# Kernel optimization log

Measured on AMD Instinct MI355X. Metric: run time of the kernel, lower is better.

Reference implementation:

```python
import jax, jax.numpy as jnp
import numpy as np
import math

B, N, DIM, H, D = 2, 2048, 1024, 16, 64
EXPECTED_K = 1.0
LAYERSCALE_INIT = 0.001
EPS = 1e-6  # flax LayerNorm default


def layer_norm(x, scale, bias):
    mu = jnp.mean(x, axis=-1, keepdims=True)
    var = jnp.mean((x - mu) ** 2, axis=-1, keepdims=True)
    return (x - mu) * jax.lax.rsqrt(var + EPS) * scale + bias


def setup_inputs() -> dict:
    key = jax.random.key(0)
    ks = jax.random.split(key, 8)
    s = DIM ** -0.5
    x = jax.random.normal(ks[0], (B, N, DIM), jnp.float32)
    Wq = jax.random.normal(ks[1], (DIM, H * D), jnp.float32) * s
    Wk = jax.random.normal(ks[2], (DIM, H * D), jnp.float32) * s
    Wv = jax.random.normal(ks[3], (DIM, H * D), jnp.float32) * s
    Wo = jax.random.normal(ks[4], (H * D, DIM), jnp.float32) * ((H * D) ** -0.5)
    e = EXPECTED_K / N
    init_bias = jnp.full((1, 1, 1, 1), math.log(e / (1.0 - e)), jnp.float32)
    return {
        'x': x,
        'Wq': Wq, 'bq': jnp.zeros((H * D,), jnp.float32),
        'Wk': Wk, 'bk': jnp.zeros((H * D,), jnp.float32),
        'Wv': Wv, 'bv': jnp.zeros((H * D,), jnp.float32),
        'qn_scale': jnp.ones((D,), jnp.float32), 'qn_bias': jnp.zeros((D,), jnp.float32),
        'kn_scale': jnp.ones((D,), jnp.float32), 'kn_bias': jnp.zeros((D,), jnp.float32),
        'init_bias': init_bias,
        'Wo': Wo, 'bo': jnp.zeros((DIM,), jnp.float32),
        'gamma': jnp.full((DIM,), LAYERSCALE_INIT, jnp.float32),
    }


def reference(x, Wq, bq, Wk, bk, Wv, bv, qn_scale, qn_bias, kn_scale, kn_bias,
              init_bias, Wo, bo, gamma):
    Bv, Nv, _ = x.shape
    q = (x @ Wq + bq).reshape(Bv, Nv, H, D)
    k = (x @ Wk + bk).reshape(Bv, Nv, H, D)
    v = (x @ Wv + bv).reshape(Bv, Nv, H, D)
    q = layer_norm(q, qn_scale, qn_bias)
    k = layer_norm(k, kn_scale, kn_bias)
    q = jnp.swapaxes(q, 1, 2)  # [B,H,N,D]
    k = jnp.swapaxes(k, 1, 2)
    v = jnp.swapaxes(v, 1, 2)
    # NOTE: original code computes scale = head_dim**-0.5 but never applies it.
    attn_logits = jnp.einsum('bhid,bhjd->bhij', q, k)
    attn_weights = jax.nn.sigmoid(attn_logits + init_bias)
    out = jnp.einsum('bhij,bhjd->bhid', attn_weights, v)
    out = jnp.swapaxes(out, 1, 2).reshape(Bv, Nv, H * D)
    out = out @ Wo + bo
    return out * gamma
```

## Files before the change

kernel.cpp:

```cpp
#include <hip/hip_runtime.h>

#define DEV static __device__ __forceinline__

typedef __bf16 bf16x8 __attribute__((ext_vector_type(8)));
typedef __bf16 bf16x4 __attribute__((ext_vector_type(4)));
typedef float f32x4 __attribute__((ext_vector_type(4)));
typedef float f32x16 __attribute__((ext_vector_type(16)));
typedef unsigned int uint4v __attribute__((ext_vector_type(4)));
typedef unsigned short ushort4v __attribute__((ext_vector_type(4)));
using u16 = unsigned short;

#define NN 2048
#define DIMD 1024

DEV u16 f2bf(float f) {
    __bf16 b = (__bf16)f;
    return __builtin_bit_cast(u16, b);
}
DEV float bf2f(u16 s) {
    unsigned u = ((unsigned)s) << 16;
    return __builtin_bit_cast(float, u);
}
DEV bf16x8 load16(const u16* p) { return __builtin_bit_cast(bf16x8, *(const uint4v*)p); }
DEV f32x4 mfma16(bf16x8 a, bf16x8 b, f32x4 c) {
    return __builtin_amdgcn_mfma_f32_16x16x32_bf16(a, b, c, 0, 0, 0);
}
DEV f32x16 mfma32(bf16x8 a, bf16x8 b, f32x16 c) {
    return __builtin_amdgcn_mfma_f32_32x32x16_bf16(a, b, c, 0, 0, 0);
}
DEV void gl_lds16(const u16* g, u16* l) {
    __builtin_amdgcn_global_load_lds((const __attribute__((address_space(1))) void*)g,
                                     (__attribute__((address_space(3))) void*)l, 16, 0, 0);
}


__global__ __launch_bounds__(256) void k_prep(const float* __restrict__ x,
                                              const float* __restrict__ s0,
                                              const float* __restrict__ s1,
                                              const float* __restrict__ s2,
                                              const float* __restrict__ s3,
                                              u16* __restrict__ xb,
                                              u16* __restrict__ wqkv_t,
                                              u16* __restrict__ wo_t) {
    __shared__ float tile[32][33];
    const int z = blockIdx.z;
    if (z < 4) {
        const float* src = (z == 0) ? s0 : (z == 1) ? s1 : (z == 2) ? s2 : s3;
        u16* dst = (z < 3) ? (wqkv_t + (size_t)z * 1024 * 1024) : wo_t;
        int tx = threadIdx.x & 31, ty = threadIdx.x >> 5;
        int kb = blockIdx.y * 32, nb = blockIdx.x * 32;
#pragma unroll
        for (int j = 0; j < 4; ++j)
            tile[ty + 8 * j][tx] = src[(size_t)(kb + ty + 8 * j) * 1024 + nb + tx];
        __syncthreads();
#pragma unroll
        for (int j = 0; j < 4; ++j)
            dst[(size_t)(nb + ty + 8 * j) * 1024 + kb + tx] = f2bf(tile[tx][ty + 8 * j]);
    } else {
        const int bidx = blockIdx.y * 32 + blockIdx.x;
#pragma unroll
        for (int q = 0; q < 4; ++q) {
            int i = bidx * 1024 + q * 256 + threadIdx.x;
            float4 v = ((const float4*)x)[i];
            ushort4v o;
            o[0] = f2bf(v.x); o[1] = f2bf(v.y); o[2] = f2bf(v.z); o[3] = f2bf(v.w);
            *(ushort4v*)(xb + (size_t)i * 4) = o;
        }
    }
}

__global__ __launch_bounds__(256) void k_gemm_qkv(const u16* __restrict__ A,
                                                  const u16* __restrict__ Bt,
                                                  const float* __restrict__ bq,
                                                  const float* __restrict__ bk,
                                                  const float* __restrict__ bv,
                                                  const float* __restrict__ qs,
                                                  const float* __restrict__ qb,
                                                  const float* __restrict__ ks,
                                                  const float* __restrict__ kb_,
                                                  u16* __restrict__ Qf,
                                                  u16* __restrict__ Kf,
                                                  u16* __restrict__ Vf) {
    __shared__ u16 As[128 * 64];
    __shared__ u16 Bs[128 * 64];
    const int K = 1024;
    const int m0 = blockIdx.x * 128, n0 = blockIdx.y * 128;
    const int tid = threadIdx.x;
    const int lane = tid & 63, w = tid >> 6;
    const int wr = w >> 1, wc = w & 1;
    const int li = lane & 15, g = lane >> 4;
    const int l7 = li & 7;

    f32x4 acc[4][4] = {};

    const int lr = lane >> 3;
    const int lc = (lane & 7) ^ lr;
    const u16* gA = A + (size_t)(m0 + w * 8 + lr) * K + lc * 8;
    const u16* gB = Bt + (size_t)(n0 + w * 8 + lr) * K + lc * 8;
    u16* lA = &As[w * 512];
    u16* lB = &Bs[w * 512];

    for (int k0 = 0; k0 < K; k0 += 64) {
        __syncthreads();
#pragma unroll
        for (int i = 0; i < 4; ++i) {
            gl_lds16(gA + (size_t)(i * 32) * K + k0, lA + i * 2048);
            gl_lds16(gB + (size_t)(i * 32) * K + k0, lB + i * 2048);
        }
        asm volatile("s_waitcnt vmcnt(0)" ::: "memory");
        __syncthreads();
        bf16x8 af[4][2], bfv[4][2];
#pragma unroll
        for (int mi = 0; mi < 4; ++mi) {
            const int row = wr * 64 + mi * 16 + li;
#pragma unroll
            for (int s = 0; s < 2; ++s)
                af[mi][s] = load16(&As[row * 64 + (((s * 4 + g) ^ l7) * 8)]);
        }
#pragma unroll
        for (int ni = 0; ni < 4; ++ni) {
            const int row = wc * 64 + ni * 16 + li;
#pragma unroll
            for (int s = 0; s < 2; ++s)
                bfv[ni][s] = load16(&Bs[row * 64 + (((s * 4 + g) ^ l7) * 8)]);
        }
#pragma unroll
        for (int mi = 0; mi < 4; ++mi)
#pragma unroll
            for (int ni = 0; ni < 4; ++ni) {
                acc[mi][ni] = mfma16(af[mi][0], bfv[ni][0], acc[mi][ni]);
                acc[mi][ni] = mfma16(af[mi][1], bfv[ni][1], acc[mi][ni]);
            }
    }

    const int col0 = n0 + wc * 64;
    const int seg = col0 >> 10;
    const int hcol = col0 & 1023;
    const int h = hcol >> 6;

    if (seg < 2) {
        const float* S = (seg == 0) ? qs : ks;
        const float* Bb = (seg == 0) ? qb : kb_;
        const float* bias = (seg == 0) ? bq : bk;
        u16* dst = (seg == 0) ? Qf : Kf;
        const float sc = (seg == 0) ? -1.44269504f : 1.0f;
        float lnS[4], lnB[4], bv4[4];
#pragma unroll
        for (int ni = 0; ni < 4; ++ni) {
            int d = ni * 16 + li;
            lnS[ni] = S[d] * sc; lnB[ni] = Bb[d] * sc; bv4[ni] = bias[hcol + d];
        }
#pragma unroll
        for (int mi = 0; mi < 4; ++mi) {
#pragma unroll
            for (int r = 0; r < 4; ++r) {
                float v0 = acc[mi][0][r] + bv4[0];
                float v1 = acc[mi][1][r] + bv4[1];
                float v2 = acc[mi][2][r] + bv4[2];
                float v3 = acc[mi][3][r] + bv4[3];
                float s1 = v0 + v1 + v2 + v3;
                float s2 = v0 * v0 + v1 * v1 + v2 * v2 + v3 * v3;
#pragma unroll
                for (int o = 1; o < 16; o <<= 1) {
                    s1 += __shfl_xor(s1, o);
                    s2 += __shfl_xor(s2, o);
                }
                float mu = s1 * (1.0f / 64.0f);
                float var = s2 * (1.0f / 64.0f) - mu * mu;
                float rsv = rsqrtf(var + 1e-6f);
                int row = m0 + wr * 64 + mi * 16 + 4 * g + r;
                int bseq = row >> 11, n = row & 2047;
                size_t base = ((size_t)(bseq * 16 + h)) * 131072 +
                              ((size_t)(n >> 5) * 4) * 512 + (size_t)(n & 31) * 8 +
                              (li >> 3) * 256 + (li & 7);
                dst[base + 0 * 512] = f2bf((v0 - mu) * rsv * lnS[0] + lnB[0]);
                dst[base + 1 * 512] = f2bf((v1 - mu) * rsv * lnS[1] + lnB[1]);
                dst[base + 2 * 512] = f2bf((v2 - mu) * rsv * lnS[2] + lnB[2]);
                dst[base + 3 * 512] = f2bf((v3 - mu) * rsv * lnS[3] + lnB[3]);
            }
        }
    } else {
        float bv4[4];
#pragma unroll
        for (int ni = 0; ni < 4; ++ni) bv4[ni] = bv[hcol + ni * 16 + li];
#pragma unroll
        for (int mi = 0; mi < 4; ++mi) {
#pragma unroll
            for (int r = 0; r < 4; ++r) {
                int row = m0 + wr * 64 + mi * 16 + 4 * g + r;
                int bseq = row >> 11, j = row & 2047;
                size_t vb_ = ((size_t)(bseq * 16 + h)) * 131072 +
                             ((size_t)((j >> 5) * 4 + ((j >> 4) & 1))) * 512 +
                             (size_t)(((j >> 3) & 1) * 32) * 8 + (j & 7);
#pragma unroll
                for (int ni = 0; ni < 4; ++ni)
                    Vf[vb_ + (ni >> 1) * 1024 + ((ni & 1) * 16 + li) * 8] =
                        f2bf(acc[mi][ni][r] + bv4[ni]);
            }
        }
    }
}

__global__ __launch_bounds__(256) void k_gemm_out(const u16* __restrict__ A,
                                                  const u16* __restrict__ Bt,
                                                  const float* __restrict__ bias,
                                                  const float* __restrict__ gamma,
                                                  float* __restrict__ out) {
    __shared__ u16 As[128 * 64];
    __shared__ u16 Bs[64 * 64];
    const int K = 1024, ldc = 1024;
    const int m0 = blockIdx.x * 128, n0 = blockIdx.y * 64;
    const int tid = threadIdx.x;
    const int lane = tid & 63, w = tid >> 6;
    const int wr = w >> 1, wc = w & 1;
    const int li = lane & 15, g = lane >> 4;
    const int l7 = li & 7;

    f32x4 acc[4][2] = {};

    const int lr = lane >> 3;
    const int lc = (lane & 7) ^ lr;
    const u16* gA = A + (size_t)(m0 + w * 8 + lr) * K + lc * 8;
    const u16* gB = Bt + (size_t)(n0 + w * 8 + lr) * K + lc * 8;
    u16* lA = &As[w * 512];
    u16* lB = &Bs[w * 512];

    for (int k0 = 0; k0 < K; k0 += 64) {
        __syncthreads();
#pragma unroll
        for (int i = 0; i < 4; ++i)
            gl_lds16(gA + (size_t)(i * 32) * K + k0, lA + i * 2048);
#pragma unroll
        for (int i = 0; i < 2; ++i)
            gl_lds16(gB + (size_t)(i * 32) * K + k0, lB + i * 2048);
        asm volatile("s_waitcnt vmcnt(0)" ::: "memory");
        __syncthreads();
        bf16x8 af[4][2], bfv[2][2];
#pragma unroll
        for (int mi = 0; mi < 4; ++mi) {
            const int row = wr * 64 + mi * 16 + li;
#pragma unroll
            for (int s = 0; s < 2; ++s)
                af[mi][s] = load16(&As[row * 64 + (((s * 4 + g) ^ l7) * 8)]);
        }
#pragma unroll
        for (int ni = 0; ni < 2; ++ni) {
            const int row = wc * 32 + ni * 16 + li;
#pragma unroll
            for (int s = 0; s < 2; ++s)
                bfv[ni][s] = load16(&Bs[row * 64 + (((s * 4 + g) ^ l7) * 8)]);
        }
#pragma unroll
        for (int mi = 0; mi < 4; ++mi)
#pragma unroll
            for (int ni = 0; ni < 2; ++ni) {
                acc[mi][ni] = mfma16(af[mi][0], bfv[ni][0], acc[mi][ni]);
                acc[mi][ni] = mfma16(af[mi][1], bfv[ni][1], acc[mi][ni]);
            }
    }

#pragma unroll
    for (int mi = 0; mi < 4; ++mi) {
        int row = m0 + wr * 64 + mi * 16 + 4 * g;
#pragma unroll
        for (int ni = 0; ni < 2; ++ni) {
            int col = n0 + wc * 32 + ni * 16 + li;
            float bv_ = bias[col], gv = gamma[col];
            f32x4 v = acc[mi][ni];
#pragma unroll
            for (int r = 0; r < 4; ++r)
                out[(size_t)(row + r) * ldc + col] = (v[r] + bv_) * gv;
        }
    }
}

__global__ __launch_bounds__(256, 2) void k_attn(const u16* __restrict__ Qf,
                                                 const u16* __restrict__ Kf,
                                                 const u16* __restrict__ Vf,
                                                 const float* __restrict__ ib,
                                                 u16* __restrict__ attn_out) {
    __shared__ float red[2][64][65];
    const int bid = blockIdx.x;
    const int xcd = bid & 7, idx = bid >> 3;
    const int bh = xcd * 4 + (idx >> 5);
    const int iblk = idx & 31;
    const int b = bh >> 4, h = bh & 15;
    const int tid = threadIdx.x;
    const int jq = tid >> 6, lane = tid & 63;
    const int l32 = lane & 31, hi = lane >> 5;
    const float c0 = -ib[0] * 1.44269504f;
    const u16* Qb = Qf + (size_t)bh * 131072;
    const u16* Kb = Kf + (size_t)bh * 131072;
    const u16* Vb = Vf + (size_t)bh * 131072;
    const int it0 = iblk * 2;

    bf16x8 qf[2][4];
#pragma unroll
    for (int t = 0; t < 2; ++t)
#pragma unroll
        for (int s = 0; s < 4; ++s)
            qf[t][s] = load16(Qb + ((size_t)((it0 + t) * 4 + s)) * 512 + lane * 8);

    f32x16 accO[2][2] = {};
    const u16* kb0 = Kb + (size_t)(jq * 16) * 2048;
    const u16* vb0 = Vb + (size_t)(jq * 16) * 2048;

    f32x16 cinit;
#pragma unroll
    for (int r = 0; r < 16; ++r) cinit[r] = c0;

    bf16x8 kf[2][4];
#pragma unroll
    for (int s = 0; s < 4; ++s) kf[0][s] = load16(kb0 + s * 512 + lane * 8);
#pragma unroll
    for (int s = 0; s < 4; ++s) kf[1][s] = load16(kb0 + 2048 + s * 512 + lane * 8);
    f32x16 sa0 = cinit, sa1;
#pragma unroll
    for (int s = 0; s < 4; ++s) sa0 = mfma32(kf[0][s], qf[0][s], sa0);

#pragma unroll 2
    for (int jt = 0; jt < 16; ++jt) {
        const int cur = jt & 1, nxt = cur ^ 1;
        bf16x8 vf[2][2];
        const u16* vbc = vb0 + (size_t)jt * 2048;
#pragma unroll
        for (int db = 0; db < 2; ++db)
#pragma unroll
            for (int js = 0; js < 2; ++js)
                vf[db][js] = load16(vbc + (db * 2 + js) * 512 + lane * 8);
        __builtin_amdgcn_s_setprio(1);
        sa1 = cinit;
#pragma unroll
        for (int s = 0; s < 4; ++s) sa1 = mfma32(kf[cur][s], qf[1][s], sa1);
        __builtin_amdgcn_s_setprio(0);
        if (jt < 14) {
            const u16* kbn = kb0 + (size_t)(jt + 2) * 2048;
#pragma unroll
            for (int s = 0; s < 4; ++s) kf[cur][s] = load16(kbn + s * 512 + lane * 8);
        }
        __builtin_amdgcn_sched_barrier(0);
        bf16x8 p00, p01;
        {
            float p[16];
#pragma unroll
            for (int r = 0; r < 16; ++r) {
                float e = __builtin_amdgcn_exp2f(sa0[r]);
                p[r] = __builtin_amdgcn_rcpf(1.0f + e);
            }
            unsigned wd[8];
#pragma unroll
            for (int u2 = 0; u2 < 8; ++u2) {
                unsigned r_;
                asm("v_cvt_pk_bf16_f32 %0, %1, %2"
                    : "=v"(r_) : "v"(p[2 * u2]), "v"(p[2 * u2 + 1]));
                wd[u2] = r_;
            }
            asm("v_permlane32_swap_b32 %0, %1" : "+v"(wd[0]), "+v"(wd[2]));
            asm("v_permlane32_swap_b32 %0, %1" : "+v"(wd[1]), "+v"(wd[3]));
            asm("v_permlane32_swap_b32 %0, %1" : "+v"(wd[4]), "+v"(wd[6]));
            asm("v_permlane32_swap_b32 %0, %1" : "+v"(wd[5]), "+v"(wd[7]));
            uint4v u0 = {wd[0], wd[1], wd[2], wd[3]};
            uint4v u1 = {wd[4], wd[5], wd[6], wd[7]};
            p00 = __builtin_bit_cast(bf16x8, u0);
            p01 = __builtin_bit_cast(bf16x8, u1);
        }
        __builtin_amdgcn_sched_barrier(0);
        __builtin_amdgcn_s_setprio(1);
        accO[0][0] = mfma32(vf[0][0], p00, accO[0][0]);
        accO[0][0] = mfma32(vf[0][1], p01, accO[0][0]);
        accO[0][1] = mfma32(vf[1][0], p00, accO[0][1]);
        accO[0][1] = mfma32(vf[1][1], p01, accO[0][1]);
        if (jt < 15) {
            sa0 = cinit;
#pragma unroll
            for (int s = 0; s < 4; ++s) sa0 = mfma32(kf[nxt][s], qf[0][s], sa0);
        }
        __builtin_amdgcn_s_setprio(0);
        __builtin_amdgcn_sched_barrier(0);
        bf16x8 p10, p11;
        {
            float p[16];
#pragma unroll
            for (int r = 0; r < 16; ++r) {
                float e = __builtin_amdgcn_exp2f(sa1[r]);
                p[r] = __builtin_amdgcn_rcpf(1.0f + e);
            }
            unsigned wd[8];
#pragma unroll
            for (int u2 = 0; u2 < 8; ++u2) {
                unsigned r_;
                asm("v_cvt_pk_bf16_f32 %0, %1, %2"
                    : "=v"(r_) : "v"(p[2 * u2]), "v"(p[2 * u2 + 1]));
                wd[u2] = r_;
            }
            asm("v_permlane32_swap_b32 %0, %1" : "+v"(wd[0]), "+v"(wd[2]));
            asm("v_permlane32_swap_b32 %0, %1" : "+v"(wd[1]), "+v"(wd[3]));
            asm("v_permlane32_swap_b32 %0, %1" : "+v"(wd[4]), "+v"(wd[6]));
            asm("v_permlane32_swap_b32 %0, %1" : "+v"(wd[5]), "+v"(wd[7]));
            uint4v u0 = {wd[0], wd[1], wd[2], wd[3]};
            uint4v u1 = {wd[4], wd[5], wd[6], wd[7]};
            p10 = __builtin_bit_cast(bf16x8, u0);
            p11 = __builtin_bit_cast(bf16x8, u1);
        }
        __builtin_amdgcn_sched_barrier(0);
        __builtin_amdgcn_s_setprio(1);
        accO[1][0] = mfma32(vf[0][0], p10, accO[1][0]);
        accO[1][0] = mfma32(vf[0][1], p11, accO[1][0]);
        accO[1][1] = mfma32(vf[1][0], p10, accO[1][1]);
        accO[1][1] = mfma32(vf[1][1], p11, accO[1][1]);
        __builtin_amdgcn_s_setprio(0);
    }

    if (jq & 1) {
#pragma unroll
        for (int t = 0; t < 2; ++t)
#pragma unroll
            for (int db = 0; db < 2; ++db)
#pragma unroll
                for (int r = 0; r < 16; ++r)
                    red[jq >> 1][t * 32 + l32][db * 32 + (r & 3) + 8 * (r >> 2) + 4 * hi] =
                        accO[t][db][r];
    }
    __syncthreads();
    if (!(jq & 1)) {
#pragma unroll
        for (int t = 0; t < 2; ++t)
#pragma unroll
            for (int db = 0; db < 2; ++db)
#pragma unroll
                for (int r = 0; r < 16; ++r)
                    accO[t][db][r] +=
                        red[jq >> 1][t * 32 + l32][db * 32 + (r & 3) + 8 * (r >> 2) + 4 * hi];
    }
    __syncthreads();
    if (jq == 2) {
#pragma unroll
        for (int t = 0; t < 2; ++t)
#pragma unroll
            for (int db = 0; db < 2; ++db)
#pragma unroll
                for (int r = 0; r < 16; ++r)
                    red[0][t * 32 + l32][db * 32 + (r & 3) + 8 * (r >> 2) + 4 * hi] =
                        accO[t][db][r];
    }
    __syncthreads();
    if (jq == 0) {
#pragma unroll
        for (int t = 0; t < 2; ++t)
#pragma unroll
            for (int db = 0; db < 2; ++db)
#pragma unroll
                for (int r = 0; r < 16; ++r)
                    accO[t][db][r] +=
                        red[0][t * 32 + l32][db * 32 + (r & 3) + 8 * (r >> 2) + 4 * hi];
#pragma unroll
        for (int t = 0; t < 2; ++t) {
            const int i = it0 * 32 + t * 32 + l32;
#pragma unroll
            for (int db = 0; db < 2; ++db)
#pragma unroll
                for (int q = 0; q < 4; ++q) {
                    int d = db * 32 + 8 * q + 4 * hi;
                    bf16x4 o4;
#pragma unroll
                    for (int r = 0; r < 4; ++r) o4[r] = (__bf16)accO[t][db][4 * q + r];
                    *(bf16x4*)&attn_out[(size_t)(b * NN + i) * 1024 + h * 64 + d] = o4;
                }
        }
    }
}


extern "C" void kernel_launch(void* const* d_in, const int* in_sizes, int n_in,
                              void* d_out, int out_size, void* d_ws, size_t ws_size,
                              hipStream_t stream) {
    (void)in_sizes; (void)n_in; (void)out_size; (void)ws_size;
    const float* x     = (const float*)d_in[0];
    const float* Wq    = (const float*)d_in[1];
    const float* bq    = (const float*)d_in[2];
    const float* Wk    = (const float*)d_in[3];
    const float* bk    = (const float*)d_in[4];
    const float* Wv    = (const float*)d_in[5];
    const float* bv    = (const float*)d_in[6];
    const float* qn_s  = (const float*)d_in[7];
    const float* qn_b  = (const float*)d_in[8];
    const float* kn_s  = (const float*)d_in[9];
    const float* kn_b  = (const float*)d_in[10];
    const float* ib    = (const float*)d_in[11];
    const float* Wo    = (const float*)d_in[12];
    const float* bo    = (const float*)d_in[13];
    const float* gamma = (const float*)d_in[14];
    float* out = (float*)d_out;

    char* ws = (char*)d_ws;
    size_t off = 0;
    auto alloc = [&](size_t bytes) -> void* {
        void* p = ws + off;
        off += (bytes + 255) & ~(size_t)255;
        return p;
    };
    u16* xb       = (u16*)alloc((size_t)4096 * 1024 * 2);
    u16* wqkv_t   = (u16*)alloc((size_t)3072 * 1024 * 2);
    u16* wo_t     = (u16*)alloc((size_t)1024 * 1024 * 2);
    u16* Qf       = (u16*)alloc((size_t)32 * 131072 * 2);
    u16* Kf       = (u16*)alloc((size_t)32 * 131072 * 2);
    u16* Vf       = (u16*)alloc((size_t)32 * 131072 * 2);
    u16* attn_out = (u16*)alloc((size_t)4096 * 1024 * 2);

    k_prep<<<dim3(32, 32, 5), 256, 0, stream>>>(x, Wq, Wk, Wv, Wo, xb, wqkv_t, wo_t);
    k_gemm_qkv<<<dim3(32, 24), 256, 0, stream>>>(xb, wqkv_t, bq, bk, bv,
                                                 qn_s, qn_b, kn_s, kn_b, Qf, Kf, Vf);
    k_attn<<<1024, 256, 0, stream>>>(Qf, Kf, Vf, ib, attn_out);
    k_gemm_out<<<dim3(32, 16), 256, 0, stream>>>(attn_out, wo_t, bo, gamma, out);
}
```

Baseline: 116.1 us.

## Double-buffer LDS tiles in QKV and output GEMMs; stagger attention waves

Both projection GEMMs now use two LDS buffers. The global-to-LDS copy for the next K-slice is issued before the MFMAs on the current slice, so memory latency overlaps with compute instead of serialising. This doubles shared memory per block (64KB for QKV, 48KB for out), which may lower occupancy. Separately, the attention kernel has odd jq waves sleep briefly before the main loop, staggering them so MFMA and load phases interleave across waves.

```diff
diff --git a/kernel.cpp b/kernel.cpp
--- a/kernel.cpp
+++ b/kernel.cpp
@@ -81,8 +81,8 @@
                                                   u16* __restrict__ Qf,
                                                   u16* __restrict__ Kf,
                                                   u16* __restrict__ Vf) {
-    __shared__ u16 As[128 * 64];
-    __shared__ u16 Bs[128 * 64];
+    __shared__ u16 As[2][128 * 64];
+    __shared__ u16 Bs[2][128 * 64];
     const int K = 1024;
     const int m0 = blockIdx.x * 128, n0 = blockIdx.y * 128;
     const int tid = threadIdx.x;
@@ -97,32 +97,41 @@
     const int lc = (lane & 7) ^ lr;
     const u16* gA = A + (size_t)(m0 + w * 8 + lr) * K + lc * 8;
     const u16* gB = Bt + (size_t)(n0 + w * 8 + lr) * K + lc * 8;
-    u16* lA = &As[w * 512];
-    u16* lB = &Bs[w * 512];
-
-    for (int k0 = 0; k0 < K; k0 += 64) {
-        __syncthreads();
+
+    auto STAGE = [&](int buf, int k0) {
+        u16* lA = &As[buf][w * 512];
+        u16* lB = &Bs[buf][w * 512];
 #pragma unroll
         for (int i = 0; i < 4; ++i) {
             gl_lds16(gA + (size_t)(i * 32) * K + k0, lA + i * 2048);
             gl_lds16(gB + (size_t)(i * 32) * K + k0, lB + i * 2048);
         }
-        asm volatile("s_waitcnt vmcnt(0)" ::: "memory");
-        __syncthreads();
+    };
+
+    STAGE(0, 0);
+    asm volatile("s_waitcnt vmcnt(0)" ::: "memory");
+    __syncthreads();
+
+    for (int t = 0; t < 16; ++t) {
+        const int cur = t & 1;
+        if (t < 15) STAGE(cur ^ 1, (t + 1) * 64);
+        __builtin_amdgcn_sched_barrier(0);
+        const u16* as = As[cur];
+        const u16* bs = Bs[cur];
         bf16x8 af[4][2], bfv[4][2];
 #pragma unroll
         for (int mi = 0; mi < 4; ++mi) {
             const int row = wr * 64 + mi * 16 + li;
 #pragma unroll
             for (int s = 0; s < 2; ++s)
-                af[mi][s] = load16(&As[row * 64 + (((s * 4 + g) ^ l7) * 8)]);
+                af[mi][s] = load16(&as[row * 64 + (((s * 4 + g) ^ l7) * 8)]);
         }
 #pragma unroll
         for (int ni = 0; ni < 4; ++ni) {
             const int row = wc * 64 + ni * 16 + li;
 #pragma unroll
             for (int s = 0; s < 2; ++s)
-                bfv[ni][s] = load16(&Bs[row * 64 + (((s * 4 + g) ^ l7) * 8)]);
+                bfv[ni][s] = load16(&bs[row * 64 + (((s * 4 + g) ^ l7) * 8)]);
         }
 #pragma unroll
         for (int mi = 0; mi < 4; ++mi)
@@ -131,6 +140,8 @@
                 acc[mi][ni] = mfma16(af[mi][0], bfv[ni][0], acc[mi][ni]);
                 acc[mi][ni] = mfma16(af[mi][1], bfv[ni][1], acc[mi][ni]);
             }
+        asm volatile("s_waitcnt vmcnt(0)" ::: "memory");
+        __syncthreads();
     }
 
     const int col0 = n0 + wc * 64;
@@ -206,8 +217,8 @@
                                                   const float* __restrict__ bias,
                                                   const float* __restrict__ gamma,
                                                   float* __restrict__ out) {
-    __shared__ u16 As[128 * 64];
-    __shared__ u16 Bs[64 * 64];
+    __shared__ u16 As[2][128 * 64];
+    __shared__ u16 Bs[2][64 * 64];
     const int K = 1024, ldc = 1024;
     const int m0 = blockIdx.x * 128, n0 = blockIdx.y * 64;
     const int tid = threadIdx.x;
@@ -222,33 +233,42 @@
     const int lc = (lane & 7) ^ lr;
     const u16* gA = A + (size_t)(m0 + w * 8 + lr) * K + lc * 8;
     const u16* gB = Bt + (size_t)(n0 + w * 8 + lr) * K + lc * 8;
-    u16* lA = &As[w * 512];
-    u16* lB = &Bs[w * 512];
-
-    for (int k0 = 0; k0 < K; k0 += 64) {
-        __syncthreads();
+
+    auto STAGE = [&](int buf, int k0) {
+        u16* lA = &As[buf][w * 512];
+        u16* lB = &Bs[buf][w * 512];
 #pragma unroll
         for (int i = 0; i < 4; ++i)
             gl_lds16(gA + (size_t)(i * 32) * K + k0, lA + i * 2048);
 #pragma unroll
         for (int i = 0; i < 2; ++i)
             gl_lds16(gB + (size_t)(i * 32) * K + k0, lB + i * 2048);
-        asm volatile("s_waitcnt vmcnt(0)" ::: "memory");
-        __syncthreads();
+    };
+
+    STAGE(0, 0);
+    asm volatile("s_waitcnt vmcnt(0)" ::: "memory");
+    __syncthreads();
+
+    for (int t = 0; t < 16; ++t) {
+        const int cur = t & 1;
+        if (t < 15) STAGE(cur ^ 1, (t + 1) * 64);
+        __builtin_amdgcn_sched_barrier(0);
+        const u16* as = As[cur];
+        const u16* bs = Bs[cur];
         bf16x8 af[4][2], bfv[2][2];
 #pragma unroll
         for (int mi = 0; mi < 4; ++mi) {
             const int row = wr * 64 + mi * 16 + li;
 #pragma unroll
             for (int s = 0; s < 2; ++s)
-                af[mi][s] = load16(&As[row * 64 + (((s * 4 + g) ^ l7) * 8)]);
+                af[mi][s] = load16(&as[row * 64 + (((s * 4 + g) ^ l7) * 8)]);
         }
 #pragma unroll
         for (int ni = 0; ni < 2; ++ni) {
             const int row = wc * 32 + ni * 16 + li;
 #pragma unroll
             for (int s = 0; s < 2; ++s)
-                bfv[ni][s] = load16(&Bs[row * 64 + (((s * 4 + g) ^ l7) * 8)]);
+                bfv[ni][s] = load16(&bs[row * 64 + (((s * 4 + g) ^ l7) * 8)]);
         }
 #pragma unroll
         for (int mi = 0; mi < 4; ++mi)
@@ -257,6 +277,8 @@
                 acc[mi][ni] = mfma16(af[mi][0], bfv[ni][0], acc[mi][ni]);
                 acc[mi][ni] = mfma16(af[mi][1], bfv[ni][1], acc[mi][ni]);
             }
+        asm volatile("s_waitcnt vmcnt(0)" ::: "memory");
+        __syncthreads();
     }
 
 #pragma unroll
@@ -317,6 +339,8 @@
     f32x16 sa0 = cinit, sa1;
 #pragma unroll
     for (int s = 0; s < 4; ++s) sa0 = mfma32(kf[0][s], qf[0][s], sa0);
+
+    if (jq & 1) __builtin_amdgcn_s_sleep(8);
 
 #pragma unroll 2
     for (int jt = 0; jt < 16; ++jt) {
```

New measurement: 117.8 us. No clear change (+1.5%).
